# Kernel tuning notes

Hardware: AMD Instinct MI355X
Metric: run time of the kernel (lower is better)

Reference implementation:

```python
import jax, jax.numpy as jnp
import numpy as np

EMBED_DIM = 1024
NUM_HEADS = 16
HEAD_DIM = EMBED_DIM // NUM_HEADS


def setup_inputs() -> dict:
    key = jax.random.key(0)
    ks = jax.random.split(key, 9)
    B, S, E = 2, 2048, EMBED_DIM
    scale = 1.0 / np.sqrt(E)
    return {
        "query": jax.random.normal(ks[0], (B, S, E), jnp.float32),
        "key": jax.random.normal(ks[1], (B, S, E), jnp.float32),
        "value": jax.random.normal(ks[2], (B, S, E), jnp.float32),
        "wq": jax.random.normal(ks[3], (E, E), jnp.float32) * scale,
        "bq": jnp.zeros((E,), jnp.float32),
        "wk": jax.random.normal(ks[4], (E, E), jnp.float32) * scale,
        "bk": jnp.zeros((E,), jnp.float32),
        "wv": jax.random.normal(ks[5], (E, E), jnp.float32) * scale,
        "bv": jnp.zeros((E,), jnp.float32),
    }


def _split_heads(x):
    B, S, _ = x.shape
    return x.reshape(B, S, NUM_HEADS, HEAD_DIM).transpose(0, 2, 1, 3)  # [B,H,S,Dh]


def reference(query, key, value, wq, bq, wk, bk, wv, bv):
    q = _split_heads(query @ wq + bq)   # [B,H,S,Dh]
    k = _split_heads(key @ wk + bk)
    v = _split_heads(value @ wv + bv)
    logits = jnp.einsum("bhqd,bhkd->bhqk", q, k) / jnp.sqrt(
        jnp.asarray(HEAD_DIM, q.dtype)
    )
    attn = jax.nn.softmax(logits, axis=-1)          # [B,H,S,S]
    out = jnp.einsum("bhqk,bhkd->bhqd", attn, v)    # [B,H,S,Dh]
    B, H, S, Dh = out.shape
    out = out.transpose(0, 2, 1, 3).reshape(B, S, H * Dh)  # [B,S,E]
    return out, attn
```

## Files before the change

kernel.cpp:

```cpp
#include <hip/hip_runtime.h>

typedef float  f32x4   __attribute__((ext_vector_type(4)));
typedef float  f32x16  __attribute__((ext_vector_type(16)));
typedef int    i32x4   __attribute__((ext_vector_type(4)));
typedef short  bf16x8  __attribute__((ext_vector_type(8)));
typedef short  s16x4   __attribute__((ext_vector_type(4)));

#define NB   2
#define SEQ  2048
#define EMB  1024
#define NH   16
#define DH   64
#define MATN (NB * SEQ * EMB)

__device__ inline short f2bf(float f) {
    unsigned u = __float_as_uint(f);
    u += 0x7fffu + ((u >> 16) & 1u);
    return (short)(u >> 16);
}

__device__ inline unsigned cvtpk(float lo, float hi) {
    unsigned r;
    asm("v_cvt_pk_bf16_f32 %0, %1, %2" : "=v"(r) : "v"(lo), "v"(hi));
    return r;
}

__device__ inline float fexp2(float x) {
#if __has_builtin(__builtin_amdgcn_exp2f)
    return __builtin_amdgcn_exp2f(x);
#else
    return exp2f(x);
#endif
}

__device__ inline f32x4 mfma16(bf16x8 a, bf16x8 b, f32x4 c) {
    return __builtin_amdgcn_mfma_f32_16x16x32_bf16(a, b, c, 0, 0, 0);
}
__device__ inline f32x16 mfma32(bf16x8 a, bf16x8 b, f32x16 c) {
    return __builtin_amdgcn_mfma_f32_32x32x16_bf16(a, b, c, 0, 0, 0);
}

__device__ inline void gload_lds16(const short* g, short* l) {
    __builtin_amdgcn_global_load_lds(
        (const __attribute__((address_space(1))) void*)g,
        (__attribute__((address_space(3))) void*)l, 16, 0, 0);
}

__global__ __launch_bounds__(256) void prep_kernel(const float* __restrict__ q,
                                                   const float* __restrict__ k,
                                                   const float* __restrict__ v,
                                                   const float* __restrict__ w0,
                                                   const float* __restrict__ w1,
                                                   const float* __restrict__ w2,
                                                   short* __restrict__ wt,
                                                   short* __restrict__ abf) {
    int blk = blockIdx.x;
    int t = threadIdx.x;
    if (blk < 3072) {
        __shared__ float tile[32][33];
        int mat = blk >> 10;
        int rem = blk & 1023;
        int kt = rem >> 5, nt = rem & 31;
        const float* W = (mat == 0) ? w0 : ((mat == 1) ? w1 : w2);
        int row = t >> 3, c4 = (t & 7) << 2;

        f32x4 val = *(const f32x4*)(W + (kt * 32 + row) * EMB + nt * 32 + c4);
        tile[row][c4 + 0] = val[0];
        tile[row][c4 + 1] = val[1];
        tile[row][c4 + 2] = val[2];
        tile[row][c4 + 3] = val[3];
        __syncthreads();

        int n = nt * 32 + row;
        s16x4 o;
        o[0] = f2bf(tile[c4 + 0][row]);
        o[1] = f2bf(tile[c4 + 1][row]);
        o[2] = f2bf(tile[c4 + 2][row]);
        o[3] = f2bf(tile[c4 + 3][row]);
        *(s16x4*)(wt + mat * (EMB * EMB) + n * EMB + kt * 32 + c4) = o;
    } else {
        long long i = (long long)(blk - 3072) * 2048 + t * 8;
        int mat = (int)(i >> 22);
        int off = (int)(i & (MATN - 1));
        const float* A = (mat == 0) ? q : ((mat == 1) ? k : v);
        f32x4 x = *(const f32x4*)(A + off);
        f32x4 y = *(const f32x4*)(A + off + 4);
        bf16x8 pk;
        pk[0] = f2bf(x[0]); pk[1] = f2bf(x[1]); pk[2] = f2bf(x[2]); pk[3] = f2bf(x[3]);
        pk[4] = f2bf(y[0]); pk[5] = f2bf(y[1]); pk[6] = f2bf(y[2]); pk[7] = f2bf(y[3]);
        *(bf16x8*)(abf + i) = pk;
    }
}

template <bool BF16A>
__global__ __launch_bounds__(256) void proj_kernel(const short* __restrict__ abf,
                                                   const float* __restrict__ a0,
                                                   const float* __restrict__ a1,
                                                   const float* __restrict__ a2,
                                                   const float* __restrict__ b0,
                                                   const float* __restrict__ b1,
                                                   const float* __restrict__ b2,
                                                   const short* __restrict__ wt,
                                                   short* __restrict__ qkv) {
    __shared__ __align__(16) short smem[18432];

    int orig = blockIdx.x;
    int blk = (orig & 7) * 96 + (orig >> 3);
    int mat = blk >> 8;
    int rem = blk & 255;
    int mt = rem >> 3, nt = rem & 7;

    const float* bias = (mat == 0) ? b0 : ((mat == 1) ? b1 : b2);
    const float* Af = (mat == 0) ? a0 : ((mat == 1) ? a1 : a2);
    const short* Ab = abf + mat * MATN;
    const short* WT = wt + mat * (EMB * EMB);
    short* O = qkv + mat * MATN;
    float scale = (mat == 0) ? 0.125f * 1.44269504f : 1.0f;

    int t = threadIdx.x;
    int lane = t & 63, w = t >> 6;
    int wr = w >> 1, wc = w & 1;
    int lg = lane >> 4, lm = lane & 15;

    int m0 = mt * 128, n0 = nt * 128;

    f32x4 acc[4][4] = {};

    if constexpr (BF16A) {
        const short* gA[4];
        const short* gW[4];
        int ldso[4];
#pragma unroll
        for (int i = 0; i < 4; i++) {
            int u = w * 256 + i * 64 + lane;
            int row = u >> 3;
            int c = (u & 7) ^ (row & 7);
            gA[i] = Ab + (m0 + row) * EMB + c * 8;
            gW[i] = WT + (n0 + row) * EMB + c * 8;
            ldso[i] = (w * 256 + i * 64) * 8;
        }
        int xr = lm & 7;
        for (int k0 = 0; k0 < EMB; k0 += 64) {
#pragma unroll
            for (int i = 0; i < 4; i++) {
                gload_lds16(gA[i] + k0, smem + ldso[i]);
                gload_lds16(gW[i] + k0, smem + 8192 + ldso[i]);
            }
            __syncthreads();
#pragma unroll
            for (int ks = 0; ks < 2; ks++) {
                bf16x8 af[4], bfr[4];
                int cc = (ks * 4 + lg) ^ xr;
#pragma unroll
                for (int mi = 0; mi < 4; mi++)
                    af[mi] = *(const bf16x8*)(smem + (wr * 64 + mi * 16 + lm) * 64 + cc * 8);
#pragma unroll
                for (int ni = 0; ni < 4; ni++)
                    bfr[ni] = *(const bf16x8*)(smem + 8192 + (wc * 64 + ni * 16 + lm) * 64 + cc * 8);
#pragma unroll
                for (int mi = 0; mi < 4; mi++)
#pragma unroll
                    for (int ni = 0; ni < 4; ni++)
                        acc[mi][ni] = mfma16(af[mi], bfr[ni], acc[mi][ni]);
            }
            __syncthreads();
        }
    } else {
        int srow = t >> 1, koff = (t & 1) * 32;
        for (int k0 = 0; k0 < EMB; k0 += 64) {
            const float* ap = Af + (m0 + srow) * EMB + k0 + koff;
#pragma unroll
            for (int i = 0; i < 4; i++) {
                f32x4 x = *(const f32x4*)(ap + i * 8);
                f32x4 y = *(const f32x4*)(ap + i * 8 + 4);
                bf16x8 pk;
                pk[0] = f2bf(x[0]); pk[1] = f2bf(x[1]); pk[2] = f2bf(x[2]); pk[3] = f2bf(x[3]);
                pk[4] = f2bf(y[0]); pk[5] = f2bf(y[1]); pk[6] = f2bf(y[2]); pk[7] = f2bf(y[3]);
                *(bf16x8*)&smem[srow * 72 + koff + i * 8] = pk;
            }
            const short* wp = WT + (n0 + srow) * EMB + k0 + koff;
#pragma unroll
            for (int i = 0; i < 4; i++)
                *(i32x4*)&smem[9216 + srow * 72 + koff + i * 8] = *(const i32x4*)(wp + i * 8);
            __syncthreads();
#pragma unroll
            for (int ks = 0; ks < 2; ks++) {
                bf16x8 af[4], bfr[4];
#pragma unroll
                for (int mi = 0; mi < 4; mi++)
                    af[mi] = *(const bf16x8*)&smem[(wr * 64 + mi * 16 + lm) * 72 + ks * 32 + lg * 8];
#pragma unroll
                for (int ni = 0; ni < 4; ni++)
                    bfr[ni] = *(const bf16x8*)&smem[9216 + (wc * 64 + ni * 16 + lm) * 72 + ks * 32 + lg * 8];
#pragma unroll
                for (int mi = 0; mi < 4; mi++)
#pragma unroll
                    for (int ni = 0; ni < 4; ni++)
                        acc[mi][ni] = mfma16(af[mi], bfr[ni], acc[mi][ni]);
            }
            __syncthreads();
        }
    }

    int bidx = m0 >> 11;
    if (mat == 2) {
#pragma unroll
        for (int ni = 0; ni < 4; ni++) {
            int e = n0 + wc * 64 + ni * 16 + lm;
            float bv = bias[e];
            int h = e >> 6, d = e & 63;
#pragma unroll
            for (int mi = 0; mi < 4; mi++) {
                int s = (m0 + wr * 64 + mi * 16 + lg * 4) & (SEQ - 1);
                s16x4 o;
#pragma unroll
                for (int r = 0; r < 4; r++) o[r] = f2bf(acc[mi][ni][r] + bv);
                *(s16x4*)(O + (((bidx * NH + h) * DH + d) * SEQ) + s) = o;
            }
        }
    } else {
#pragma unroll
        for (int ni = 0; ni < 4; ni++) {
            int e = n0 + wc * 64 + ni * 16 + lm;
            float bv = bias[e];
#pragma unroll
            for (int mi = 0; mi < 4; mi++) {
                int rr = wr * 64 + mi * 16 + lg * 4;
#pragma unroll
                for (int r = 0; r < 4; r++)
                    smem[(rr + r) * 136 + wc * 64 + ni * 16 + lm] =
                        f2bf((acc[mi][ni][r] + bv) * scale);
            }
        }
        __syncthreads();
        int r = t >> 1, half = t & 1;
        int h = (n0 + half * 64) >> 6;
        int s = (m0 + r) & (SEQ - 1);
        short* dst = O + (((long long)bidx * NH + h) * SEQ + s) * DH;
        const short* srcp = smem + r * 136 + half * 64;
#pragma unroll
        for (int j = 0; j < 8; j++)
            *(i32x4*)(dst + j * 8) = *(const i32x4*)(srcp + j * 8);
    }
}

__global__ __launch_bounds__(256) void attn_kernel(const short* __restrict__ qkv,
                                                   float* __restrict__ out,
                                                   float* __restrict__ attn) {
    const short* Qb = qkv;
    const short* Kb = qkv + MATN;
    const short* Vt = qkv + 2 * MATN;

    __shared__ __align__(16) short kbuf[2][64][72];
    __shared__ __align__(16) short vbuf[2][4096];
    __shared__ float lds_rs[4][32];

    int orig = blockIdx.x;
    int wg = (orig & 7) * 128 + (orig >> 3);
    int bh = wg >> 5;
    int q0 = (wg & 31) * 64;
    int b = bh >> 4, hq = bh & 15;

    int t = threadIdx.x, lane = t & 63, w = t >> 6;
    int lg = lane >> 4, lm = lane & 15;
    int srow = t >> 2, sch = t & 3;

    const short* kbase = Kb + (long long)bh * SEQ * DH;
    const short* vbase = Vt + (long long)bh * DH * SEQ;

    bf16x8 qf0, qf1;
    {
        const short* qrow = Qb + ((long long)bh * SEQ + q0 + w * 16 + lm) * DH + lg * 8;
        qf0 = *(const bf16x8*)(qrow);
        qf1 = *(const bf16x8*)(qrow + 32);
    }

    int l31 = lane & 31, l5 = lane >> 5;
    int khalf = w >> 1;
    bf16x8 qw[4];
    {
        const short* qr = Qb + ((long long)bh * SEQ + q0 + (w & 1) * 32 + l31) * DH + l5 * 8;
        qw[0] = *(const bf16x8*)(qr);
        qw[1] = *(const bf16x8*)(qr + 16);
        qw[2] = *(const bf16x8*)(qr + 32);
        qw[3] = *(const bf16x8*)(qr + 48);
    }

    i32x4 kr0, kr1;
    {
        const short* kp = kbase + srow * DH + sch * 16;
        kr0 = *(const i32x4*)(kp); kr1 = *(const i32x4*)(kp + 8);
    }
    float rsum = 0.0f;
    for (int kt = 0; kt < 32; kt++) {
        *(i32x4*)&kbuf[kt & 1][srow][sch * 16]     = kr0;
        *(i32x4*)&kbuf[kt & 1][srow][sch * 16 + 8] = kr1;
        __syncthreads();
        if (kt < 31) {
            const short* kp = kbase + ((kt + 1) * 64 + srow) * DH + sch * 16;
            kr0 = *(const i32x4*)(kp); kr1 = *(const i32x4*)(kp + 8);
        }
        const short* kb = &kbuf[kt & 1][khalf * 32 + l31][l5 * 8];
        f32x16 s = {};
        __builtin_amdgcn_s_setprio(1);
        s = mfma32(*(const bf16x8*)(kb),      qw[0], s);
        s = mfma32(*(const bf16x8*)(kb + 16), qw[1], s);
        s = mfma32(*(const bf16x8*)(kb + 32), qw[2], s);
        s = mfma32(*(const bf16x8*)(kb + 48), qw[3], s);
        __builtin_amdgcn_s_setprio(0);
#pragma unroll
        for (int r = 0; r < 16; r++) rsum += fexp2(s[r]);
    }
    rsum += __shfl_xor(rsum, 32);
    if (lane < 32) lds_rs[w][lane] = rsum;
    __syncthreads();
    float ml2r;
    {
        int q = w * 16 + lm;
        float tot = (q < 32) ? (lds_rs[0][q] + lds_rs[2][q])
                             : (lds_rs[1][q - 32] + lds_rs[3][q - 32]);
        ml2r = -__log2f(tot);
    }

    f32x4 oacc[4] = {};
    float* arow = attn + ((long long)bh * SEQ + q0 + w * 16 + lm) * SEQ;

    int vA0 = (srow >> 4) * 1024 + (sch >> 1) * 512 + (srow & 15) * 8 + (sch & 1) * 4;

    i32x4 vr0, vr1;
    {
        const short* kp = kbase + srow * DH + sch * 16;
        kr0 = *(const i32x4*)(kp); kr1 = *(const i32x4*)(kp + 8);
        const short* vp = vbase + srow * SEQ + sch * 16;
        vr0 = *(const i32x4*)(vp); vr1 = *(const i32x4*)(vp + 8);
    }

    for (int kt = 0; kt < 32; kt++) {
        *(i32x4*)&kbuf[kt & 1][srow][sch * 16]     = kr0;
        *(i32x4*)&kbuf[kt & 1][srow][sch * 16 + 8] = kr1;
        union { i32x4 v; s16x4 h[2]; } u0, u1;
        u0.v = vr0; u1.v = vr1;
        *(s16x4*)&vbuf[kt & 1][vA0]       = u0.h[0];
        *(s16x4*)&vbuf[kt & 1][vA0 + 128] = u0.h[1];
        *(s16x4*)&vbuf[kt & 1][vA0 + 256] = u1.h[0];
        *(s16x4*)&vbuf[kt & 1][vA0 + 384] = u1.h[1];
        __syncthreads();
        if (kt < 31) {
            const short* kp = kbase + ((kt + 1) * 64 + srow) * DH + sch * 16;
            kr0 = *(const i32x4*)(kp); kr1 = *(const i32x4*)(kp + 8);
            const short* vp = vbase + srow * SEQ + (kt + 1) * 64 + sch * 16;
            vr0 = *(const i32x4*)(vp); vr1 = *(const i32x4*)(vp + 8);
        }

        float p[4][4];
#pragma unroll
        for (int ki = 0; ki < 4; ki++) {
            f32x4 s = {ml2r, ml2r, ml2r, ml2r};
            bf16x8 kf0 = *(const bf16x8*)&kbuf[kt & 1][ki * 16 + lm][lg * 8];
            bf16x8 kf1 = *(const bf16x8*)&kbuf[kt & 1][ki * 16 + lm][32 + lg * 8];
            __builtin_amdgcn_s_setprio(1);
            s = mfma16(kf0, qf0, s);
            s = mfma16(kf1, qf1, s);
            __builtin_amdgcn_s_setprio(0);
#pragma unroll
            for (int r = 0; r < 4; r++) p[ki][r] = fexp2(s[r]);
            f32x4 st = {p[ki][0], p[ki][1], p[ki][2], p[ki][3]};
            *(f32x4*)(arow + kt * 64 + ki * 16 + lg * 4) = st;
        }

        bf16x8 pb[2];
#pragma unroll
        for (int ks = 0; ks < 2; ks++) {
            union { unsigned d[4]; bf16x8 v; } up;
            up.d[0] = cvtpk(p[2 * ks + 0][0], p[2 * ks + 0][1]);
            up.d[1] = cvtpk(p[2 * ks + 0][2], p[2 * ks + 0][3]);
            up.d[2] = cvtpk(p[2 * ks + 1][0], p[2 * ks + 1][1]);
            up.d[3] = cvtpk(p[2 * ks + 1][2], p[2 * ks + 1][3]);
            pb[ks] = up.v;
        }

        __builtin_amdgcn_s_setprio(1);
#pragma unroll
        for (int di = 0; di < 4; di++) {
#pragma unroll
            for (int ks = 0; ks < 2; ks++) {
                bf16x8 vf = *(const bf16x8*)&vbuf[kt & 1][(di * 2 + ks) * 512 + (lg * 16 + lm) * 8];
                oacc[di] = mfma16(vf, pb[ks], oacc[di]);
            }
        }
        __builtin_amdgcn_s_setprio(0);
    }

    float* op = out + ((long long)b * SEQ + q0 + w * 16 + lm) * EMB + hq * DH;
#pragma unroll
    for (int di = 0; di < 4; di++) {
        __builtin_nontemporal_store(oacc[di], (f32x4*)(op + di * 16 + lg * 4));
    }
}

extern "C" void kernel_launch(void* const* d_in, const int* in_sizes, int n_in,
                              void* d_out, int out_size, void* d_ws, size_t ws_size,
                              hipStream_t stream) {
    const float* query = (const float*)d_in[0];
    const float* key   = (const float*)d_in[1];
    const float* value = (const float*)d_in[2];
    const float* wq    = (const float*)d_in[3];
    const float* bq    = (const float*)d_in[4];
    const float* wk    = (const float*)d_in[5];
    const float* bk    = (const float*)d_in[6];
    const float* wv    = (const float*)d_in[7];
    const float* bv    = (const float*)d_in[8];

    float* out  = (float*)d_out;
    float* attn = out + (long long)NB * SEQ * EMB;

    size_t need_full = ((size_t)3 * EMB * EMB + 6ull * MATN) * sizeof(short);
    bool bf16a = ws_size >= need_full;

    short* wt  = (short*)d_ws;
    short* abf = wt + 3 * (EMB * EMB);
    short* qkv = bf16a ? (abf + 3 * MATN) : abf;

    hipLaunchKernelGGL(prep_kernel, dim3(bf16a ? 9216 : 3072), dim3(256), 0, stream,
                       query, key, value, wq, wk, wv, wt, abf);
    if (bf16a) {
        hipLaunchKernelGGL((proj_kernel<true>), dim3(768), dim3(256), 0, stream,
                           abf, query, key, value, bq, bk, bv, wt, qkv);
    } else {
        hipLaunchKernelGGL((proj_kernel<false>), dim3(768), dim3(256), 0, stream,
                           abf, query, key, value, bq, bk, bv, wt, qkv);
    }
    hipLaunchKernelGGL(attn_kernel, dim3(1024), dim3(256), 0, stream,
                       qkv, out, attn);
}
```

Before: 243.0 us.

## Split softmax row-sum pass into separate highly parallel kernel over key chunks

Moves the first pass (computing exp row sums of QK^T) out of the attention kernel into a new rsum_kernel that splits the key dimension into 16 chunks of 128 and launches 8192 blocks, writing partial sums to workspace. The attention kernel then reads and adds the 16 partials before the second pass, removing its serial 32-iteration K loop. This raises parallelism for the first pass but adds a kernel launch, extra workspace traffic, and recomputation of Q loads across chunks. The workspace layout is reordered so the partial sums sit before the optional bf16 activation buffer.

```diff
diff --git a/kernel.cpp b/kernel.cpp
--- a/kernel.cpp
+++ b/kernel.cpp
@@ -12,6 +12,8 @@
 #define NH   16
 #define DH   64
 #define MATN (NB * SEQ * EMB)
+#define NBH  (NB * NH)
+#define KC   16
 
 __device__ inline short f2bf(float f) {
     unsigned u = __float_as_uint(f);
@@ -244,63 +246,46 @@
     }
 }
 
-__global__ __launch_bounds__(256) void attn_kernel(const short* __restrict__ qkv,
-                                                   float* __restrict__ out,
-                                                   float* __restrict__ attn) {
+__global__ __launch_bounds__(256) void rsum_kernel(const short* __restrict__ qkv,
+                                                   float* __restrict__ rs) {
     const short* Qb = qkv;
     const short* Kb = qkv + MATN;
-    const short* Vt = qkv + 2 * MATN;
-
-    __shared__ __align__(16) short kbuf[2][64][72];
-    __shared__ __align__(16) short vbuf[2][4096];
-    __shared__ float lds_rs[4][32];
+
+    __shared__ __align__(16) short kbuf[128][72];
 
     int orig = blockIdx.x;
-    int wg = (orig & 7) * 128 + (orig >> 3);
-    int bh = wg >> 5;
-    int q0 = (wg & 31) * 64;
-    int b = bh >> 4, hq = bh & 15;
+    int wg = (orig & 7) * 1024 + (orig >> 3);
+    int bh = wg >> 8;
+    int rem = wg & 255;
+    int qt = rem >> 4, kc = rem & 15;
+    int q0 = qt * 128, k0 = kc * 128;
 
     int t = threadIdx.x, lane = t & 63, w = t >> 6;
-    int lg = lane >> 4, lm = lane & 15;
-    int srow = t >> 2, sch = t & 3;
-
-    const short* kbase = Kb + (long long)bh * SEQ * DH;
-    const short* vbase = Vt + (long long)bh * DH * SEQ;
-
-    bf16x8 qf0, qf1;
+    int l31 = lane & 31, l5 = lane >> 5;
+
     {
-        const short* qrow = Qb + ((long long)bh * SEQ + q0 + w * 16 + lm) * DH + lg * 8;
-        qf0 = *(const bf16x8*)(qrow);
-        qf1 = *(const bf16x8*)(qrow + 32);
-    }
-
-    int l31 = lane & 31, l5 = lane >> 5;
-    int khalf = w >> 1;
+        int row = t >> 2, sc = t & 3;
+#pragma unroll
+        for (int rr = 0; rr < 2; rr++) {
+            const short* kp = Kb + ((long long)bh * SEQ + k0 + rr * 64 + row) * DH + sc * 16;
+            *(i32x4*)&kbuf[rr * 64 + row][sc * 16]     = *(const i32x4*)(kp);
+            *(i32x4*)&kbuf[rr * 64 + row][sc * 16 + 8] = *(const i32x4*)(kp + 8);
+        }
+    }
     bf16x8 qw[4];
     {
-        const short* qr = Qb + ((long long)bh * SEQ + q0 + (w & 1) * 32 + l31) * DH + l5 * 8;
+        const short* qr = Qb + ((long long)bh * SEQ + q0 + w * 32 + l31) * DH + l5 * 8;
         qw[0] = *(const bf16x8*)(qr);
         qw[1] = *(const bf16x8*)(qr + 16);
         qw[2] = *(const bf16x8*)(qr + 32);
         qw[3] = *(const bf16x8*)(qr + 48);
     }
-
-    i32x4 kr0, kr1;
-    {
-        const short* kp = kbase + srow * DH + sch * 16;
-        kr0 = *(const i32x4*)(kp); kr1 = *(const i32x4*)(kp + 8);
-    }
+    __syncthreads();
+
     float rsum = 0.0f;
-    for (int kt = 0; kt < 32; kt++) {
-        *(i32x4*)&kbuf[kt & 1][srow][sch * 16]     = kr0;
-        *(i32x4*)&kbuf[kt & 1][srow][sch * 16 + 8] = kr1;
-        __syncthreads();
-        if (kt < 31) {
-            const short* kp = kbase + ((kt + 1) * 64 + srow) * DH + sch * 16;
-            kr0 = *(const i32x4*)(kp); kr1 = *(const i32x4*)(kp + 8);
-        }
-        const short* kb = &kbuf[kt & 1][khalf * 32 + l31][l5 * 8];
+#pragma unroll
+    for (int ks = 0; ks < 4; ks++) {
+        const short* kb = &kbuf[ks * 32 + l31][l5 * 8];
         f32x16 s = {};
         __builtin_amdgcn_s_setprio(1);
         s = mfma32(*(const bf16x8*)(kb),      qw[0], s);
@@ -312,13 +297,48 @@
         for (int r = 0; r < 16; r++) rsum += fexp2(s[r]);
     }
     rsum += __shfl_xor(rsum, 32);
-    if (lane < 32) lds_rs[w][lane] = rsum;
-    __syncthreads();
+    if (lane < 32)
+        rs[((long long)kc * NBH + bh) * SEQ + q0 + w * 32 + lane] = rsum;
+}
+
+__global__ __launch_bounds__(256) void attn_kernel(const short* __restrict__ qkv,
+                                                   const float* __restrict__ rs,
+                                                   float* __restrict__ out,
+                                                   float* __restrict__ attn) {
+    const short* Qb = qkv;
+    const short* Kb = qkv + MATN;
+    const short* Vt = qkv + 2 * MATN;
+
+    __shared__ __align__(16) short kbuf[2][64][72];
+    __shared__ __align__(16) short vbuf[2][4096];
+
+    int orig = blockIdx.x;
+    int wg = (orig & 7) * 128 + (orig >> 3);
+    int bh = wg >> 5;
+    int q0 = (wg & 31) * 64;
+    int b = bh >> 4, hq = bh & 15;
+
+    int t = threadIdx.x, lane = t & 63, w = t >> 6;
+    int lg = lane >> 4, lm = lane & 15;
+    int srow = t >> 2, sch = t & 3;
+
+    const short* kbase = Kb + (long long)bh * SEQ * DH;
+    const short* vbase = Vt + (long long)bh * DH * SEQ;
+
+    bf16x8 qf0, qf1;
+    {
+        const short* qrow = Qb + ((long long)bh * SEQ + q0 + w * 16 + lm) * DH + lg * 8;
+        qf0 = *(const bf16x8*)(qrow);
+        qf1 = *(const bf16x8*)(qrow + 32);
+    }
+
     float ml2r;
     {
-        int q = w * 16 + lm;
-        float tot = (q < 32) ? (lds_rs[0][q] + lds_rs[2][q])
-                             : (lds_rs[1][q - 32] + lds_rs[3][q - 32]);
+        const float* rp = rs + (long long)bh * SEQ + q0 + w * 16 + lm;
+        float tot = 0.0f;
+#pragma unroll
+        for (int kc = 0; kc < KC; kc++)
+            tot += rp[(long long)kc * (NBH * SEQ)];
         ml2r = -__log2f(tot);
     }
 
@@ -327,7 +347,7 @@
 
     int vA0 = (srow >> 4) * 1024 + (sch >> 1) * 512 + (srow & 15) * 8 + (sch & 1) * 4;
 
-    i32x4 vr0, vr1;
+    i32x4 kr0, kr1, vr0, vr1;
     {
         const short* kp = kbase + srow * DH + sch * 16;
         kr0 = *(const i32x4*)(kp); kr1 = *(const i32x4*)(kp + 8);
@@ -414,12 +434,17 @@
     float* out  = (float*)d_out;
     float* attn = out + (long long)NB * SEQ * EMB;
 
-    size_t need_full = ((size_t)3 * EMB * EMB + 6ull * MATN) * sizeof(short);
+    size_t wtN  = (size_t)3 * EMB * EMB;
+    size_t qkvN = (size_t)3 * MATN;
+    size_t rsN  = (size_t)KC * NBH * SEQ;
+    size_t need_base = (wtN + qkvN) * 2 + rsN * 4;
+    size_t need_full = need_base + (size_t)3 * MATN * 2;
     bool bf16a = ws_size >= need_full;
 
     short* wt  = (short*)d_ws;
-    short* abf = wt + 3 * (EMB * EMB);
-    short* qkv = bf16a ? (abf + 3 * MATN) : abf;
+    short* qkv = wt + wtN;
+    float* rs  = (float*)(qkv + qkvN);
+    short* abf = (short*)(rs + rsN);
 
     hipLaunchKernelGGL(prep_kernel, dim3(bf16a ? 9216 : 3072), dim3(256), 0, stream,
                        query, key, value, wq, wk, wv, wt, abf);
@@ -430,6 +455,7 @@
         hipLaunchKernelGGL((proj_kernel<false>), dim3(768), dim3(256), 0, stream,
                            abf, query, key, value, bq, bk, bv, wt, qkv);
     }
+    hipLaunchKernelGGL(rsum_kernel, dim3(8192), dim3(256), 0, stream, qkv, rs);
     hipLaunchKernelGGL(attn_kernel, dim3(1024), dim3(256), 0, stream,
-                       qkv, out, attn);
-}
+                       qkv, rs, out, attn);
+}
```

After: 257.3 us. +5.9%, slower.
